# Kernel optimization log

Hardware: AMD Instinct MI355X
Metric: run time of the kernel (lower is better)

Reference implementation:

```python
import jax, jax.numpy as jnp
import numpy as np

B, S, D = 2, 2048, 2048
N_HEADS = 16
HEAD_DIM = D // N_HEADS  # 128


def apply_rotary(xq, xk, cos, sin):
    # xq, xk: [B, S, H, HD]; cos, sin: [S, HD//2]
    def rot(t):
        tr = t.reshape(t.shape[:-1] + (HEAD_DIM // 2, 2))
        r, i = tr[..., 0], tr[..., 1]
        c = cos[None, :, None, :]  # [1, S, 1, HD//2]
        s = sin[None, :, None, :]
        out_r = r * c - i * s
        out_i = r * s + i * c
        return jnp.stack([out_r, out_i], axis=-1).reshape(t.shape)
    return rot(xq), rot(xk)


def setup_inputs() -> dict:
    key = jax.random.key(0)
    k1, k2, k3 = jax.random.split(key, 3)
    x = jax.random.normal(k1, (B, S, D), dtype=jnp.float32)
    wqkv = jax.random.normal(k2, (3 * D, D), dtype=jnp.float32) * (D ** -0.5)
    wo = jax.random.normal(k3, (D, D), dtype=jnp.float32) * (D ** -0.5)
    # rotary tables, standard llama theta=10000
    inv_freq = 1.0 / (10000.0 ** (jnp.arange(0, HEAD_DIM, 2, dtype=jnp.float32) / HEAD_DIM))
    t = jnp.arange(S, dtype=jnp.float32)
    freqs = jnp.outer(t, inv_freq)  # [S, HD//2]
    freqs_cos = jnp.cos(freqs)
    freqs_sin = jnp.sin(freqs)
    # causal additive mask [1, 1, S, S]
    causal = jnp.tril(jnp.ones((S, S), dtype=bool))
    mask = jnp.where(causal, 0.0, -jnp.inf).astype(jnp.float32)[None, None]
    return {"x": x, "freqs_cos": freqs_cos, "freqs_sin": freqs_sin,
            "mask": mask, "wqkv": wqkv, "wo": wo, "input_pos": 0}


def reference(x, freqs_cos, freqs_sin, mask, wqkv, wo, input_pos):
    # fused QKV projection (Linear: x @ W^T)
    qkv = jnp.einsum('bsd,ed->bse', x, wqkv)  # [B, S, 3D]
    xq, xk, xv = jnp.split(qkv, 3, axis=-1)
    xq = xq.reshape(B, S, N_HEADS, HEAD_DIM)
    xk = xk.reshape(B, S, N_HEADS, HEAD_DIM)
    xv = xv.reshape(B, S, N_HEADS, HEAD_DIM)
    xq, xk = apply_rotary(xq, xk, freqs_cos, freqs_sin)
    # SDPA (kv_cache is None; input_pos unused)
    scale = HEAD_DIM ** -0.5
    scores = jnp.einsum('bqhd,bkhd->bhqk', xq, xk) * scale + mask
    attn = jax.nn.softmax(scores, axis=-1)
    out = jnp.einsum('bhqk,bkhd->bqhd', attn, xv).reshape(B, S, D)
    return jnp.einsum('bsd,ed->bse', out, wo)
```

## Files before the change

### kernel.cpp

```cpp
#include <hip/hip_runtime.h>

#define B_ 2
#define S_ 2048
#define D_ 2048
#define H_ 16
#define DH_ 128

#define AS1 __attribute__((address_space(1)))
#define AS3 __attribute__((address_space(3)))

typedef __attribute__((ext_vector_type(4))) float f32x4;
typedef __attribute__((ext_vector_type(8))) short bf16x8;

__device__ __forceinline__ unsigned short f2bf(float f) {
  unsigned u = __float_as_uint(f);
  u += 0x7fff + ((u >> 16) & 1);
  return (unsigned short)(u >> 16);
}
__device__ __forceinline__ float bf2f(unsigned short h) {
  return __uint_as_float(((unsigned)h) << 16);
}
__device__ __forceinline__ unsigned cvt_pk_bf16(float lo, float hi) {
  unsigned r;
  asm("v_cvt_pk_bf16_f32 %0, %1, %2" : "=v"(r) : "v"(lo), "v"(hi));
  return r;
}

__global__ __launch_bounds__(256) void cast3(const float* __restrict__ x,
                                             const float* __restrict__ wq,
                                             const float* __restrict__ wo,
                                             unsigned short* __restrict__ xb,
                                             unsigned short* __restrict__ wqb,
                                             unsigned short* __restrict__ wob) {
  int i = blockIdx.x * 256 + threadIdx.x;
  const float* src; unsigned short* dst; int off;
  if (i < 2097152)      { src = x;  dst = xb;  off = i; }
  else if (i < 5242880) { src = wq; dst = wqb; off = i - 2097152; }
  else                  { src = wo; dst = wob; off = i - 5242880; }
  float4 v = reinterpret_cast<const float4*>(src)[off];
  ushort4 o;
  o.x = f2bf(v.x); o.y = f2bf(v.y); o.z = f2bf(v.z); o.w = f2bf(v.w);
  reinterpret_cast<ushort4*>(dst)[off] = o;
}

__global__ __launch_bounds__(512) void gemm_qkv256(const unsigned short* __restrict__ A,
                                                   const unsigned short* __restrict__ Bm,
                                                   unsigned short* __restrict__ qkv,
                                                   unsigned short* __restrict__ Vt) {
  __shared__ __align__(16) unsigned short As[2][256*64];
  __shared__ __align__(16) unsigned short Bs[2][192*64];
  const int t = threadIdx.x;
  const int lane = t & 63;
  const int w = t >> 6;
  const int wr = w >> 2, wc = w & 3;
  const int l16 = lane & 15, lg = lane >> 4;
  const int bm = blockIdx.y, bn = blockIdx.x;

  f32x4 acc[8][3] = {};

#define STG1(KT)                                                                                   \
  {                                                                                                \
    const int k0s = (KT) * 64;                                                                     \
    const int bufs = (KT) & 1;                                                                     \
    _Pragma("unroll")                                                                              \
    for (int rr = 0; rr < 4; ++rr) {                                                               \
      int e = t*8 + rr*4096;                                                                       \
      int row = e >> 6, g = (e >> 3) & 7, gs = g ^ (row & 7);                                      \
      const unsigned short* ga = A + (size_t)(bm*256 + row)*2048 + k0s + gs*8;                     \
      __builtin_amdgcn_global_load_lds((const AS1 unsigned int*)ga,                                \
                                       (AS3 unsigned int*)(&As[bufs][e]), 16, 0, 0);               \
    }                                                                                              \
    _Pragma("unroll")                                                                              \
    for (int rr = 0; rr < 3; ++rr) {                                                               \
      int e = t*8 + rr*4096;                                                                       \
      int row = e >> 6, g = (e >> 3) & 7, gs = g ^ (row & 7);                                      \
      const unsigned short* gb = Bm + (size_t)(bn*192 + row)*2048 + k0s + gs*8;                    \
      __builtin_amdgcn_global_load_lds((const AS1 unsigned int*)gb,                                \
                                       (AS3 unsigned int*)(&Bs[bufs][e]), 16, 0, 0);               \
    }                                                                                              \
  }

  STG1(0);
  STG1(1);

  for (int kt = 0; kt < 32; ++kt) {
    const int buf = kt & 1;
    if (kt == 31) { asm volatile("s_waitcnt vmcnt(0)" ::: "memory"); }
    else          { asm volatile("s_waitcnt vmcnt(7)" ::: "memory"); }
    __builtin_amdgcn_s_barrier();
    __builtin_amdgcn_sched_barrier(0);
    bf16x8 a0[8], b0[3];
#pragma unroll
    for (int ni = 0; ni < 3; ++ni) {
      int row = wc*48 + ni*16 + l16;
      b0[ni] = *reinterpret_cast<const bf16x8*>(&Bs[buf][row*64 + ((lg ^ (row & 7))<<3)]);
    }
#pragma unroll
    for (int m8 = 0; m8 < 8; ++m8) {
      int row = wr*128 + m8*16 + l16;
      a0[m8] = *reinterpret_cast<const bf16x8*>(&As[buf][row*64 + ((lg ^ (row & 7))<<3)]);
    }
    asm volatile("s_waitcnt lgkmcnt(0)" ::: "memory");
    __builtin_amdgcn_sched_barrier(0);
    bf16x8 a1[8], b1[3];
#pragma unroll
    for (int ni = 0; ni < 3; ++ni) {
      int row = wc*48 + ni*16 + l16;
      int g = 4 + lg;
      b1[ni] = *reinterpret_cast<const bf16x8*>(&Bs[buf][row*64 + ((g ^ (row & 7))<<3)]);
    }
#pragma unroll
    for (int m8 = 0; m8 < 8; ++m8) {
      int row = wr*128 + m8*16 + l16;
      int g = 4 + lg;
      a1[m8] = *reinterpret_cast<const bf16x8*>(&As[buf][row*64 + ((g ^ (row & 7))<<3)]);
    }
    __builtin_amdgcn_sched_barrier(0);
    __builtin_amdgcn_s_setprio(1);
#pragma unroll
    for (int m8 = 0; m8 < 8; ++m8)
#pragma unroll
      for (int ni = 0; ni < 3; ++ni)
        acc[m8][ni] = __builtin_amdgcn_mfma_f32_16x16x32_bf16(a0[m8], b0[ni], acc[m8][ni], 0, 0, 0);
    __builtin_amdgcn_s_setprio(0);
    asm volatile("s_waitcnt lgkmcnt(0)" ::: "memory");
    __builtin_amdgcn_sched_barrier(0);
    __builtin_amdgcn_s_barrier();
    if (kt < 30) STG1(kt + 2);
    __builtin_amdgcn_s_setprio(1);
#pragma unroll
    for (int m8 = 0; m8 < 8; ++m8)
#pragma unroll
      for (int ni = 0; ni < 3; ++ni)
        acc[m8][ni] = __builtin_amdgcn_mfma_f32_16x16x32_bf16(a1[m8], b1[ni], acc[m8][ni], 0, 0, 0);
    __builtin_amdgcn_s_setprio(0);
  }
#undef STG1

#pragma unroll
  for (int mi = 0; mi < 8; ++mi) {
#pragma unroll
    for (int ni = 0; ni < 3; ++ni) {
      int col = bn*192 + wc*48 + ni*16 + l16;
      int row0 = bm*256 + wr*128 + mi*16 + lg*4;
      if (col < 4096) {
#pragma unroll
        for (int r = 0; r < 4; ++r)
          qkv[(size_t)(row0 + r)*4096 + col] = f2bf(acc[mi][ni][r]);
      } else {
        int colv = col - 4096;
        int h = colv >> 7, d = colv & 127;
        int b = row0 >> 11, s = row0 & 2047;
        ushort4 v4;
        v4.x = f2bf(acc[mi][ni][0]);
        v4.y = f2bf(acc[mi][ni][1]);
        v4.z = f2bf(acc[mi][ni][2]);
        v4.w = f2bf(acc[mi][ni][3]);
        *reinterpret_cast<ushort4*>(&Vt[(((size_t)(b*H_ + h))*DH_ + d)*S_ + s]) = v4;
      }
    }
  }
}

__global__ __launch_bounds__(256) void gemm_bt(const unsigned short* __restrict__ A,
                                               const unsigned short* __restrict__ Bm,
                                               float* __restrict__ C,
                                               int Ndim, int Kdim) {
  __shared__ __align__(16) unsigned short As[2][128*64];
  __shared__ __align__(16) unsigned short Bs[2][128*64];
  const int t = threadIdx.x;
  const int lane = t & 63;
  const int w = t >> 6;
  const int wm = w >> 1, wn = w & 1;
  const int l16 = lane & 15, lg = lane >> 4;
  const int bm = blockIdx.y, bn = blockIdx.x;
  const int nkt = Kdim >> 6;

  f32x4 acc[4][4] = {};

#define STG2(KT)                                                                                   \
  {                                                                                                \
    const int k0s = (KT) * 64;                                                                     \
    const int bufs = (KT) & 1;                                                                     \
    _Pragma("unroll")                                                                              \
    for (int it = 0; it < 4; ++it) {                                                               \
      int e = t*8 + it*2048;                                                                       \
      int row = e >> 6, g = (e >> 3) & 7, gs = g ^ (row & 7);                                      \
      const unsigned short* ga = A  + (size_t)(bm*128 + row)*Kdim + k0s + gs*8;                    \
      const unsigned short* gb = Bm + (size_t)(bn*128 + row)*Kdim + k0s + gs*8;                    \
      __builtin_amdgcn_global_load_lds((const AS1 unsigned int*)ga,                                \
                                       (AS3 unsigned int*)(&As[bufs][e]), 16, 0, 0);               \
      __builtin_amdgcn_global_load_lds((const AS1 unsigned int*)gb,                                \
                                       (AS3 unsigned int*)(&Bs[bufs][e]), 16, 0, 0);               \
    }                                                                                              \
  }

  STG2(0);
  STG2(1);

  for (int kt = 0; kt < nkt; ++kt) {
    const int buf = kt & 1;
    if (kt == nkt - 1) { asm volatile("s_waitcnt vmcnt(0)" ::: "memory"); }
    else               { asm volatile("s_waitcnt vmcnt(8)" ::: "memory"); }
    __builtin_amdgcn_s_barrier();
    __builtin_amdgcn_sched_barrier(0);
    bf16x8 a0[4], b0[4];
#pragma unroll
    for (int mi = 0; mi < 4; ++mi) {
      int rowa = wm*64 + mi*16 + l16;
      a0[mi] = *reinterpret_cast<const bf16x8*>(&As[buf][rowa*64 + ((lg ^ (rowa & 7))<<3)]);
      int rowb = wn*64 + mi*16 + l16;
      b0[mi] = *reinterpret_cast<const bf16x8*>(&Bs[buf][rowb*64 + ((lg ^ (rowb & 7))<<3)]);
    }
    asm volatile("s_waitcnt lgkmcnt(0)" ::: "memory");
    __builtin_amdgcn_sched_barrier(0);
    bf16x8 a1[4], b1[4];
#pragma unroll
    for (int mi = 0; mi < 4; ++mi) {
      int g = 4 + lg;
      int rowa = wm*64 + mi*16 + l16;
      a1[mi] = *reinterpret_cast<const bf16x8*>(&As[buf][rowa*64 + ((g ^ (rowa & 7))<<3)]);
      int rowb = wn*64 + mi*16 + l16;
      b1[mi] = *reinterpret_cast<const bf16x8*>(&Bs[buf][rowb*64 + ((g ^ (rowb & 7))<<3)]);
    }
    __builtin_amdgcn_sched_barrier(0);
    __builtin_amdgcn_s_setprio(1);
#pragma unroll
    for (int mi = 0; mi < 4; ++mi)
#pragma unroll
      for (int ni = 0; ni < 4; ++ni)
        acc[mi][ni] = __builtin_amdgcn_mfma_f32_16x16x32_bf16(a0[mi], b0[ni], acc[mi][ni], 0, 0, 0);
    __builtin_amdgcn_s_setprio(0);
    asm volatile("s_waitcnt lgkmcnt(0)" ::: "memory");
    __builtin_amdgcn_sched_barrier(0);
    __builtin_amdgcn_s_barrier();
    if (kt < nkt - 2) STG2(kt + 2);
    __builtin_amdgcn_s_setprio(1);
#pragma unroll
    for (int mi = 0; mi < 4; ++mi)
#pragma unroll
      for (int ni = 0; ni < 4; ++ni)
        acc[mi][ni] = __builtin_amdgcn_mfma_f32_16x16x32_bf16(a1[mi], b1[ni], acc[mi][ni], 0, 0, 0);
    __builtin_amdgcn_s_setprio(0);
  }
#undef STG2

#pragma unroll
  for (int mi = 0; mi < 4; ++mi) {
#pragma unroll
    for (int ni = 0; ni < 4; ++ni) {
      int col = bn*128 + wn*64 + ni*16 + l16;
      int row0 = bm*128 + wm*64 + mi*16 + lg*4;
#pragma unroll
      for (int r = 0; r < 4; ++r)
        C[(size_t)(row0 + r) * Ndim + col] = acc[mi][ni][r];
    }
  }
}

__global__ __launch_bounds__(256) void rope_qk(const unsigned short* __restrict__ qkv,
                                               const float* __restrict__ cosT,
                                               const float* __restrict__ sinT,
                                               unsigned short* __restrict__ Q,
                                               unsigned short* __restrict__ K) {
  const float SCLQ = 0.08838834764831845f * 1.4426950408889634f;
  const int idx = blockIdx.x;
  const int b = idx >> 11, s = idx & 2047;
  const int t = threadIdx.x;
  const int e = t * 8;
  const int h = e >> 7, d0 = e & 127;
  const int j0 = d0 >> 1;
  const size_t rowb = (size_t)(b*S_ + s) * 4096;
  float4 c4 = *reinterpret_cast<const float4*>(&cosT[s*64 + j0]);
  float4 s4 = *reinterpret_cast<const float4*>(&sinT[s*64 + j0]);
  float cc[4] = {c4.x, c4.y, c4.z, c4.w};
  float ss[4] = {s4.x, s4.y, s4.z, s4.w};
  const size_t qo = (((size_t)(b*H_ + h)) * S_ + s) * DH_ + d0;

  ushort4 qv[2], kv[2], qd[2], kd[2];
  qv[0] = *reinterpret_cast<const ushort4*>(&qkv[rowb + e]);
  qv[1] = *reinterpret_cast<const ushort4*>(&qkv[rowb + e + 4]);
  kv[0] = *reinterpret_cast<const ushort4*>(&qkv[rowb + 2048 + e]);
  kv[1] = *reinterpret_cast<const ushort4*>(&qkv[rowb + 2048 + e + 4]);
#pragma unroll
  for (int p = 0; p < 4; ++p) {
    unsigned short* qi = (unsigned short*)&qv[p >> 1] + (p & 1) * 2;
    unsigned short* ki = (unsigned short*)&kv[p >> 1] + (p & 1) * 2;
    unsigned short* qo2 = (unsigned short*)&qd[p >> 1] + (p & 1) * 2;
    unsigned short* ko2 = (unsigned short*)&kd[p >> 1] + (p & 1) * 2;
    float x0 = bf2f(qi[0]), x1 = bf2f(qi[1]);
    qo2[0] = f2bf((x0*cc[p] - x1*ss[p]) * SCLQ);
    qo2[1] = f2bf((x0*ss[p] + x1*cc[p]) * SCLQ);
    float y0 = bf2f(ki[0]), y1 = bf2f(ki[1]);
    ko2[0] = f2bf(y0*cc[p] - y1*ss[p]);
    ko2[1] = f2bf(y0*ss[p] + y1*cc[p]);
  }
  *reinterpret_cast<ushort4*>(&Q[qo])     = qd[0];
  *reinterpret_cast<ushort4*>(&Q[qo + 4]) = qd[1];
  *reinterpret_cast<ushort4*>(&K[qo])     = kd[0];
  *reinterpret_cast<ushort4*>(&K[qo + 4]) = kd[1];
}

#define NQT 32
__global__ __launch_bounds__(512) void attn(const unsigned short* __restrict__ Q,
                                            const unsigned short* __restrict__ K,
                                            const unsigned short* __restrict__ Vt,
                                            unsigned short* __restrict__ O) {
  __shared__ __align__(16) unsigned short Ks[2][64*128];
  __shared__ __align__(16) unsigned short Vs[2][128*64];
  __shared__ __align__(16) unsigned short Plds[8][16*64];
  const int orig = blockIdx.y * gridDim.x + blockIdx.x;
  const int wgid = (orig & 7) * 64 + (orig >> 3);
  const int x = wgid & 15;
  const int bh = wgid >> 4;
  const int b = bh >> 4, h = bh & 15;
  const int t = threadIdx.x;
  const int lane = t & 63;
  const int w = t >> 6;
  const int wg8 = w >> 2;
  const int wi = w & 3;
  const int l16 = lane & 15, lg = lane >> 4;
  const int qt = wg8 ? (NQT - 1 - x) : x;
  const int q0 = qt * 64 + wi * 16;
  const unsigned short* Qh = Q  + (size_t)bh * S_ * DH_;
  const unsigned short* Kh = K  + (size_t)bh * S_ * DH_;
  const unsigned short* Vh = Vt + (size_t)bh * DH_ * S_;

  bf16x8 aq[4];
#pragma unroll
  for (int kk = 0; kk < 4; ++kk)
    aq[kk] = *reinterpret_cast<const bf16x8*>(Qh + (size_t)(q0 + l16)*DH_ + kk*32 + lg*8);

  f32x4 o[8] = {};
  float mrun = -1e30f, lrun = 0.f;
  const int ntiles = NQT - x;

#define STAGE_KV(TILE)                                                                              \
  {                                                                                                 \
    const int kv0s = (TILE) * 64;                                                                   \
    unsigned short* Kd = &Ks[(TILE) & 1][0];                                                        \
    unsigned short* Vd = &Vs[(TILE) & 1][0];                                                        \
    _Pragma("unroll")                                                                               \
    for (int it = 0; it < 2; ++it) {                                                                \
      int e = t*8 + it*4096;                                                                        \
      int row = e >> 7;                                                                             \
      int gslot = (e >> 3) & 15;                                                                    \
      int gsrc = gslot ^ (row & 7);                                                                 \
      const unsigned short* ga = Kh + (size_t)(kv0s + row) * DH_ + gsrc*8;                          \
      __builtin_amdgcn_global_load_lds((const AS1 unsigned int*)ga,                                 \
                                       (AS3 unsigned int*)(&Kd[e]), 16, 0, 0);                      \
    }                                                                                               \
    _Pragma("unroll")                                                                               \
    for (int it = 0; it < 2; ++it) {                                                                \
      int e = t*8 + it*4096;                                                                        \
      int dd = e >> 6;                                                                              \
      int gslot = (e >> 3) & 7;                                                                     \
      int gsrc = gslot ^ (dd & 7);                                                                  \
      const unsigned short* gv = Vh + (size_t)dd * S_ + kv0s + gsrc*8;                              \
      __builtin_amdgcn_global_load_lds((const AS1 unsigned int*)gv,                                 \
                                       (AS3 unsigned int*)(&Vd[e]), 16, 0, 0);                      \
    }                                                                                               \
  }

  STAGE_KV(0);

  for (int tile = 0; tile < ntiles; ++tile) {
    __syncthreads();
    if (tile + 1 < ntiles) STAGE_KV(tile + 1);
    const int kv0 = tile * 64;
    const int buf = tile & 1;

    if (tile <= qt) {
      f32x4 sc[4] = {};
      __builtin_amdgcn_s_setprio(1);
#pragma unroll
      for (int kk = 0; kk < 4; ++kk) {
#pragma unroll
        for (int n = 0; n < 4; ++n) {
          int row = n*16 + l16;
          int g = kk*4 + lg;
          bf16x8 bk = *reinterpret_cast<const bf16x8*>(&Ks[buf][row*128 + ((g ^ (row & 7))<<3)]);
          sc[n] = __builtin_amdgcn_mfma_f32_16x16x32_bf16(bk, aq[kk], sc[n], 0, 0, 0);
        }
      }
      __builtin_amdgcn_s_setprio(0);
      if (tile == qt) {
        int qrow = q0 + l16;
#pragma unroll
        for (int n = 0; n < 4; ++n)
#pragma unroll
          for (int r = 0; r < 4; ++r) {
            int kidx = kv0 + n*16 + lg*4 + r;
            sc[n][r] = (kidx > qrow) ? -1e30f : sc[n][r];
          }
      }
      float mt = sc[0][0];
#pragma unroll
      for (int n = 0; n < 4; ++n)
#pragma unroll
        for (int r = 0; r < 4; ++r) mt = fmaxf(mt, sc[n][r]);
      mt = fmaxf(mt, __shfl_xor(mt, 16));
      mt = fmaxf(mt, __shfl_xor(mt, 32));
      if (__any(mt > mrun + 8.f)) {
        float mnew = fmaxf(mrun, mt);
        float alpha = __builtin_amdgcn_exp2f(mrun - mnew);
        mrun = mnew;
        lrun *= alpha;
        float ar[4];
#pragma unroll
        for (int r = 0; r < 4; ++r) ar[r] = __shfl(alpha, lg*4 + r);
#pragma unroll
        for (int n2 = 0; n2 < 8; ++n2)
#pragma unroll
          for (int r = 0; r < 4; ++r) o[n2][r] *= ar[r];
      }
      float rs = 0.f;
      unsigned pk[4][2];
#pragma unroll
      for (int n = 0; n < 4; ++n) {
        float p0 = __builtin_amdgcn_exp2f(sc[n][0] - mrun);
        float p1 = __builtin_amdgcn_exp2f(sc[n][1] - mrun);
        float p2 = __builtin_amdgcn_exp2f(sc[n][2] - mrun);
        float p3 = __builtin_amdgcn_exp2f(sc[n][3] - mrun);
        rs += (p0 + p1) + (p2 + p3);
        pk[n][0] = cvt_pk_bf16(p0, p1);
        pk[n][1] = cvt_pk_bf16(p2, p3);
      }
      rs += __shfl_xor(rs, 16);
      rs += __shfl_xor(rs, 32);
      lrun += rs;
      unsigned short* Pw = &Plds[w][0];
      char* Pb = (char*)Pw + l16*128;
#pragma unroll
      for (int n = 0; n < 4; ++n) {
        int sslot = (n*4 + lg) ^ (l16 & 14);
        *reinterpret_cast<uint2*>(Pb + sslot*8) = make_uint2(pk[n][0], pk[n][1]);
      }
      bf16x8 pa[2];
#pragma unroll
      for (int kk2 = 0; kk2 < 2; ++kk2) {
        int tp = (kk2*4 + lg) ^ ((l16 >> 1) & 7);
        pa[kk2] = *reinterpret_cast<const bf16x8*>(Pb + tp*16);
      }
      __builtin_amdgcn_s_setprio(1);
#pragma unroll
      for (int kk2 = 0; kk2 < 2; ++kk2) {
#pragma unroll
        for (int n2 = 0; n2 < 8; ++n2) {
          int d = n2*16 + l16;
          int g = kk2*4 + lg;
          bf16x8 bv = *reinterpret_cast<const bf16x8*>(&Vs[buf][d*64 + ((g ^ (d & 7))<<3)]);
          o[n2] = __builtin_amdgcn_mfma_f32_16x16x32_bf16(pa[kk2], bv, o[n2], 0, 0, 0);
        }
      }
      __builtin_amdgcn_s_setprio(0);
    }
  }
  float linv = 1.f / lrun;
  float lr[4];
#pragma unroll
  for (int r = 0; r < 4; ++r) lr[r] = __shfl(linv, lg*4 + r);
  size_t ob = ((size_t)b * S_) * D_;
#pragma unroll
  for (int n2 = 0; n2 < 8; ++n2) {
#pragma unroll
    for (int r = 0; r < 4; ++r) {
      int rowq = q0 + lg*4 + r;
      int d = n2*16 + l16;
      O[ob + (size_t)rowq * D_ + h*DH_ + d] = f2bf(o[n2][r] * lr[r]);
    }
  }
}

extern "C" void kernel_launch(void* const* d_in, const int* in_sizes, int n_in,
                              void* d_out, int out_size, void* d_ws, size_t ws_size,
                              hipStream_t stream) {
  const float* x    = (const float*)d_in[0];
  const float* fcos = (const float*)d_in[1];
  const float* fsin = (const float*)d_in[2];
  const float* wqkv = (const float*)d_in[4];
  const float* wo   = (const float*)d_in[5];
  float* out = (float*)d_out;
  char* ws = (char*)d_ws;

  unsigned short* xb    = (unsigned short*)(ws);
  unsigned short* wqkvb = (unsigned short*)(ws + 16777216);
  unsigned short* wob   = (unsigned short*)(ws + 41943040);
  unsigned short* qkv   = (unsigned short*)(ws + 50331648);
  unsigned short* Qb    = (unsigned short*)(ws + 83886080);
  unsigned short* Kb    = (unsigned short*)(ws + 100663296);
  unsigned short* Vtb   = (unsigned short*)(ws + 117440512);
  unsigned short* attn_out = xb;

  cast3<<<dim3(24576), 256, 0, stream>>>(x, wqkv, wo, xb, wqkvb, wob);

  gemm_qkv256<<<dim3(32, 16), 512, 0, stream>>>(xb, wqkvb, qkv, Vtb);
  rope_qk<<<dim3(4096), 256, 0, stream>>>(qkv, fcos, fsin, Qb, Kb);
  attn<<<dim3(16, 32), 512, 0, stream>>>(Qb, Kb, Vtb, attn_out);
  gemm_bt<<<dim3(16, 32), 256, 0, stream>>>(attn_out, wob, out, 2048, 2048);
}
```

Before: 232.0 us.

## Restructure QKV GEMM main loop into 8-phase ping-pong schedule with split loads

Rewrites the QKV projection GEMM K-loop as an unrolled 8-phase schedule per two K-tiles. Each phase reads half of the A fragments, issues a slice of the global-to-LDS prefetch, syncs with a barrier and runs 12 MFMAs. A tiles are now loaded in two M-halves so prefetch of the next tile can start while the current buffer is still being consumed. The goal is to interleave memory traffic with MFMA work more finely and cut fragment register pressure, at the cost of many more barriers and trickier vmcnt accounting.

```diff
diff --git a/kernel.cpp b/kernel.cpp
--- a/kernel.cpp
+++ b/kernel.cpp
@@ -58,84 +58,95 @@
 
   f32x4 acc[8][3] = {};
 
-#define STG1(KT)                                                                                   \
+#define GL_A(T, MH)                                                                                \
   {                                                                                                \
-    const int k0s = (KT) * 64;                                                                     \
-    const int bufs = (KT) & 1;                                                                     \
     _Pragma("unroll")                                                                              \
-    for (int rr = 0; rr < 4; ++rr) {                                                               \
-      int e = t*8 + rr*4096;                                                                       \
-      int row = e >> 6, g = (e >> 3) & 7, gs = g ^ (row & 7);                                      \
-      const unsigned short* ga = A + (size_t)(bm*256 + row)*2048 + k0s + gs*8;                     \
+    for (int r2 = 0; r2 < 2; ++r2) {                                                               \
+      int el = t*8 + r2*4096;                                                                      \
+      int rsub = el >> 6;                                                                          \
+      int row = ((rsub >> 6) << 7) + (MH)*64 + (rsub & 63);                                        \
+      int g = (el >> 3) & 7, gs = g ^ (row & 7);                                                   \
+      const unsigned short* ga = A + (size_t)(bm*256 + row)*2048 + (T)*64 + gs*8;                  \
       __builtin_amdgcn_global_load_lds((const AS1 unsigned int*)ga,                                \
-                                       (AS3 unsigned int*)(&As[bufs][e]), 16, 0, 0);               \
+          (AS3 unsigned int*)(&As[(T) & 1][row*64 + g*8]), 16, 0, 0);                              \
+    }                                                                                              \
+  }
+#define GL_B(T)                                                                                    \
+  {                                                                                                \
+    _Pragma("unroll")                                                                              \
+    for (int r3 = 0; r3 < 3; ++r3) {                                                               \
+      int el = t*8 + r3*4096;                                                                      \
+      int row = el >> 6;                                                                           \
+      int g = (el >> 3) & 7, gs = g ^ (row & 7);                                                   \
+      const unsigned short* gb = Bm + (size_t)(bn*192 + row)*2048 + (T)*64 + gs*8;                 \
+      __builtin_amdgcn_global_load_lds((const AS1 unsigned int*)gb,                                \
+          (AS3 unsigned int*)(&Bs[(T) & 1][el]), 16, 0, 0);                                        \
+    }                                                                                              \
+  }
+
+#define PHASE_CORE(TBUF, KK, MH, BREAD, ...)                                                       \
+  {                                                                                                \
+    bf16x8 afr[4];                                                                                 \
+    if (BREAD) {                                                                                   \
+      _Pragma("unroll")                                                                            \
+      for (int ni = 0; ni < 3; ++ni) {                                                             \
+        int row = wc*48 + ni*16 + l16;                                                             \
+        int g = (KK)*4 + lg;                                                                       \
+        bfr[ni] = *reinterpret_cast<const bf16x8*>(&Bs[TBUF][row*64 + ((g ^ (row & 7)) << 3)]);    \
+      }                                                                                            \
     }                                                                                              \
     _Pragma("unroll")                                                                              \
-    for (int rr = 0; rr < 3; ++rr) {                                                               \
-      int e = t*8 + rr*4096;                                                                       \
-      int row = e >> 6, g = (e >> 3) & 7, gs = g ^ (row & 7);                                      \
-      const unsigned short* gb = Bm + (size_t)(bn*192 + row)*2048 + k0s + gs*8;                    \
-      __builtin_amdgcn_global_load_lds((const AS1 unsigned int*)gb,                                \
-                                       (AS3 unsigned int*)(&Bs[bufs][e]), 16, 0, 0);               \
+    for (int m4 = 0; m4 < 4; ++m4) {                                                               \
+      int row = wr*128 + (MH)*64 + m4*16 + l16;                                                    \
+      int g = (KK)*4 + lg;                                                                         \
+      afr[m4] = *reinterpret_cast<const bf16x8*>(&As[TBUF][row*64 + ((g ^ (row & 7)) << 3)]);      \
     }                                                                                              \
-  }
-
-  STG1(0);
-  STG1(1);
-
-  for (int kt = 0; kt < 32; ++kt) {
-    const int buf = kt & 1;
-    if (kt == 31) { asm volatile("s_waitcnt vmcnt(0)" ::: "memory"); }
-    else          { asm volatile("s_waitcnt vmcnt(7)" ::: "memory"); }
-    __builtin_amdgcn_s_barrier();
-    __builtin_amdgcn_sched_barrier(0);
-    bf16x8 a0[8], b0[3];
-#pragma unroll
-    for (int ni = 0; ni < 3; ++ni) {
-      int row = wc*48 + ni*16 + l16;
-      b0[ni] = *reinterpret_cast<const bf16x8*>(&Bs[buf][row*64 + ((lg ^ (row & 7))<<3)]);
-    }
-#pragma unroll
-    for (int m8 = 0; m8 < 8; ++m8) {
-      int row = wr*128 + m8*16 + l16;
-      a0[m8] = *reinterpret_cast<const bf16x8*>(&As[buf][row*64 + ((lg ^ (row & 7))<<3)]);
-    }
-    asm volatile("s_waitcnt lgkmcnt(0)" ::: "memory");
-    __builtin_amdgcn_sched_barrier(0);
-    bf16x8 a1[8], b1[3];
-#pragma unroll
-    for (int ni = 0; ni < 3; ++ni) {
-      int row = wc*48 + ni*16 + l16;
-      int g = 4 + lg;
-      b1[ni] = *reinterpret_cast<const bf16x8*>(&Bs[buf][row*64 + ((g ^ (row & 7))<<3)]);
-    }
-#pragma unroll
-    for (int m8 = 0; m8 < 8; ++m8) {
-      int row = wr*128 + m8*16 + l16;
-      int g = 4 + lg;
-      a1[m8] = *reinterpret_cast<const bf16x8*>(&As[buf][row*64 + ((g ^ (row & 7))<<3)]);
-    }
-    __builtin_amdgcn_sched_barrier(0);
-    __builtin_amdgcn_s_setprio(1);
-#pragma unroll
-    for (int m8 = 0; m8 < 8; ++m8)
-#pragma unroll
-      for (int ni = 0; ni < 3; ++ni)
-        acc[m8][ni] = __builtin_amdgcn_mfma_f32_16x16x32_bf16(a0[m8], b0[ni], acc[m8][ni], 0, 0, 0);
-    __builtin_amdgcn_s_setprio(0);
-    asm volatile("s_waitcnt lgkmcnt(0)" ::: "memory");
-    __builtin_amdgcn_sched_barrier(0);
-    __builtin_amdgcn_s_barrier();
-    if (kt < 30) STG1(kt + 2);
-    __builtin_amdgcn_s_setprio(1);
-#pragma unroll
-    for (int m8 = 0; m8 < 8; ++m8)
-#pragma unroll
-      for (int ni = 0; ni < 3; ++ni)
-        acc[m8][ni] = __builtin_amdgcn_mfma_f32_16x16x32_bf16(a1[m8], b1[ni], acc[m8][ni], 0, 0, 0);
-    __builtin_amdgcn_s_setprio(0);
-  }
-#undef STG1
+    __VA_ARGS__;                                                                                   \
+    __builtin_amdgcn_s_barrier();                                                                  \
+    asm volatile("s_waitcnt lgkmcnt(0)" ::: "memory");                                             \
+    __builtin_amdgcn_sched_barrier(0);                                                             \
+    __builtin_amdgcn_s_setprio(1);                                                                 \
+    _Pragma("unroll")                                                                              \
+    for (int m4 = 0; m4 < 4; ++m4)                                                                 \
+      _Pragma("unroll")                                                                            \
+      for (int ni = 0; ni < 3; ++ni)                                                               \
+        acc[(MH)*4 + m4][ni] =                                                                     \
+            __builtin_amdgcn_mfma_f32_16x16x32_bf16(afr[m4], bfr[ni], acc[(MH)*4 + m4][ni], 0, 0, 0); \
+    __builtin_amdgcn_s_setprio(0);                                                                 \
+  }
+
+#define PHASE_N(TBUF, KK, MH, BREAD, ...)                                                          \
+  PHASE_CORE(TBUF, KK, MH, BREAD, __VA_ARGS__)                                                     \
+  __builtin_amdgcn_s_barrier();
+
+#define PHASE_V(TBUF, KK, MH, BREAD, ST, ...)                                                      \
+  PHASE_CORE(TBUF, KK, MH, BREAD, __VA_ARGS__)                                                     \
+  if (ST) { asm volatile("s_waitcnt vmcnt(2)" ::: "memory"); }                                     \
+  else    { asm volatile("s_waitcnt vmcnt(0)" ::: "memory"); }                                     \
+  __builtin_amdgcn_s_barrier();
+
+  GL_A(0, 0); GL_A(0, 1); GL_B(0); GL_A(1, 0);
+  asm volatile("s_waitcnt vmcnt(2)" ::: "memory");
+  __builtin_amdgcn_s_barrier();
+
+  for (int i = 0; i < 16; ++i) {
+    const int e = 2*i, o = 2*i + 1;
+    const bool st = (i < 15);
+    bf16x8 bfr[3];
+    PHASE_N(0, 0, 0, true,  GL_B(o))
+    PHASE_N(0, 0, 1, false, GL_A(o, 1))
+    PHASE_N(0, 1, 0, true,  (void)0)
+    PHASE_V(0, 1, 1, false, st, if (st) GL_A(e + 2, 0))
+    PHASE_N(1, 0, 0, true,  if (st) GL_A(e + 2, 1))
+    PHASE_N(1, 0, 1, false, if (st) GL_B(e + 2))
+    PHASE_N(1, 1, 0, true,  (void)0)
+    PHASE_V(1, 1, 1, false, st, if (st) GL_A(o + 2, 0))
+  }
+#undef GL_A
+#undef GL_B
+#undef PHASE_CORE
+#undef PHASE_N
+#undef PHASE_V
 
 #pragma unroll
   for (int mi = 0; mi < 8; ++mi) {
```

Result: no change. 236.4 us (+1.9%).
